# Kernel optimization log

Measured on AMD Instinct MI355X. Metric: run time of the kernel, lower is better.

## Reference

```python
import jax, jax.numpy as jnp
import numpy as np

B, N, E, F = 4, 4096, 65536, 128


def setup_inputs() -> dict:
    key = jax.random.key(0)
    ks = jax.random.split(key, 16)
    s = 0.02
    inp = {
        'node_feats': jax.random.normal(ks[0], (B, N, F), jnp.float32),
        'edge_feats': jax.random.normal(ks[1], (B, E, F), jnp.float32),
        'i': jax.random.randint(ks[2], (E,), 0, N, jnp.int32),
        'j': jax.random.randint(ks[3], (E,), 0, N, jnp.int32),
        'W_src_gate': jax.random.normal(ks[4], (F, F), jnp.float32) * s,
        'b_src_gate': jnp.zeros((F,), jnp.float32),
        'W_dst_gate': jax.random.normal(ks[5], (F, F), jnp.float32) * s,
        'b_dst_gate': jnp.zeros((F,), jnp.float32),
        'W_edge_gate': jax.random.normal(ks[6], (F, F), jnp.float32) * s,
        'b_edge_gate': jnp.zeros((F,), jnp.float32),
        'W_src_update': jax.random.normal(ks[7], (F, F), jnp.float32) * s,
        'b_src_update': jnp.zeros((F,), jnp.float32),
        'W_dst_update': jax.random.normal(ks[8], (F, F), jnp.float32) * s,
        'b_dst_update': jnp.zeros((F,), jnp.float32),
    }
    return inp


def _linear(x, W, b):
    # torch nn.Linear: x @ W.T + b, W is [out, in]
    return jnp.einsum('bnf,gf->bng', x, W) + b


def reference(node_feats, edge_feats, i, j,
              W_src_gate, b_src_gate, W_dst_gate, b_dst_gate,
              W_edge_gate, b_edge_gate, W_src_update, b_src_update,
              W_dst_update, b_dst_update):
    Bn, Nn, Fn = node_feats.shape
    e_src = _linear(node_feats, W_src_gate, b_src_gate)[:, i]      # [B, E, F]
    e_dst = _linear(node_feats, W_dst_gate, b_dst_gate)[:, j]      # [B, E, F]
    y = e_src + e_dst + _linear(edge_feats, W_edge_gate, b_edge_gate)
    sigma = jax.nn.sigmoid(y)
    bh = _linear(node_feats, W_dst_update, b_dst_update)[:, j]     # [B, E, F]
    m = bh * sigma
    # scatter-add over edges into destination nodes (along dim 1)
    zeros = jnp.zeros((Bn, Nn, Fn), node_feats.dtype)
    sum_sigma_h = zeros.at[:, i].add(m)
    sum_sigma = zeros.at[:, i].add(sigma)
    h = sum_sigma_h / (sum_sigma + 1e-6)
    x = jax.nn.silu(_linear(node_feats, W_src_update, b_src_update) + h)
    y = jax.nn.silu(y)
    # residual=True
    x = node_feats + x
    y = edge_feats + y
    return (x, y)
```

## Files before the change

kernel.cpp:

```cpp
#include <hip/hip_runtime.h>
#include <hip/hip_bf16.h>

typedef __attribute__((ext_vector_type(8))) short short8;
typedef __attribute__((ext_vector_type(4))) float f32x4;
typedef __attribute__((ext_vector_type(2))) float f32x2;

#define DEVI __device__ __forceinline__

static constexpr int NB = 4;
static constexpr int NN = 4096;
static constexpr int NE = 65536;
static constexpr int MROWS = NB * NN;

DEVI short f2b(float f) {
    __hip_bfloat16 h = __float2bfloat16(f);
    return *reinterpret_cast<short*>(&h);
}
DEVI float b2f(ushort u) {
    uint v = (uint)u << 16;
    float f;
    __builtin_memcpy(&f, &v, 4);
    return f;
}

__global__ void prep_weights(const float* __restrict__ w0, const float* __restrict__ w1,
                             const float* __restrict__ w2, const float* __restrict__ w3,
                             const float* __restrict__ w4, ushort* __restrict__ out) {
    int idx = blockIdx.x * 256 + threadIdx.x;
    int wsel = idx >> 14;
    int off = idx & 16383;
    const float* src = wsel == 0 ? w0 : wsel == 1 ? w1 : wsel == 2 ? w2 : wsel == 3 ? w3 : w4;
    out[idx] = (ushort)f2b(src[off]);
}

__global__ void hist_kernel(const int* __restrict__ iIdx, int* __restrict__ cnt) {
    int e = blockIdx.x * 256 + threadIdx.x;
    atomicAdd(&cnt[iIdx[e]], 1);
}

__global__ __launch_bounds__(256) void scan_kernel(const int* __restrict__ cnt,
                                                   int* __restrict__ start) {
    __shared__ int ls[256];
    int t = threadIdx.x;
    int base = t * 16;
    int loc[16];
    int s = 0;
#pragma unroll
    for (int q = 0; q < 16; ++q) { loc[q] = s; s += cnt[base + q]; }
    ls[t] = s;
    __syncthreads();
    for (int off = 1; off < 256; off <<= 1) {
        int v = (t >= off) ? ls[t - off] : 0;
        __syncthreads();
        ls[t] += v;
        __syncthreads();
    }
    int ex = ls[t] - s;
#pragma unroll
    for (int q = 0; q < 16; ++q) start[base + q] = ex + loc[q];
    if (t == 255) start[4096] = ex + s;
}

__global__ void scatter_kernel(const int* __restrict__ iIdx, const int* __restrict__ jIdx,
                               const int* __restrict__ start, int* __restrict__ cur,
                               int* __restrict__ rank, int* __restrict__ jsort) {
    int e = blockIdx.x * 256 + threadIdx.x;
    int iv = iIdx[e];
    int pos = start[iv] + atomicAdd(&cur[iv], 1);
    rank[e] = pos;
    jsort[pos] = jIdx[e];
}

DEVI void stage_W256(const ushort* __restrict__ Wg, ushort* Wl, int tid) {
    int n = tid >> 1;
    int kh = (tid & 1) * 64;
#pragma unroll
    for (int c = 0; c < 8; ++c) {
        int k = kh + c * 8;
        short8 v = *reinterpret_cast<const short8*>(Wg + n * 128 + k);
        int byt = (n * 256 + k * 2) ^ ((n & 7) << 4);
        *reinterpret_cast<short8*>(reinterpret_cast<char*>(Wl) + byt) = v;
    }
}

DEVI void stage_W512(const ushort* __restrict__ Wg, ushort* Wl, int tid) {
    int n = tid >> 2;
    int kq = (tid & 3) * 32;
#pragma unroll
    for (int c = 0; c < 4; ++c) {
        int k = kq + c * 8;
        short8 v = *reinterpret_cast<const short8*>(Wg + n * 128 + k);
        int byt = (n * 256 + k * 2) ^ ((n & 7) << 4);
        *reinterpret_cast<short8*>(reinterpret_cast<char*>(Wl) + byt) = v;
    }
}

DEVI void load_afrag(const float* __restrict__ rowptr, int kgrp, short8 afrag[4]) {
#pragma unroll
    for (int ks = 0; ks < 4; ++ks) {
        int k0 = ks * 32 + kgrp * 8;
        f32x4 lo = *reinterpret_cast<const f32x4*>(rowptr + k0);
        f32x4 hi = *reinterpret_cast<const f32x4*>(rowptr + k0 + 4);
        short8 a;
#pragma unroll
        for (int q = 0; q < 4; ++q) a[q] = f2b(lo[q]);
#pragma unroll
        for (int q = 0; q < 4; ++q) a[4 + q] = f2b(hi[q]);
        afrag[ks] = a;
    }
}

DEVI void mfma_frags(const short8 afrag[4], const ushort* __restrict__ Wl,
                     int lane, f32x4 acc[8]) {
    const int colb = lane & 15;
    const int kgrp = lane >> 4;
#pragma unroll
    for (int nt = 0; nt < 8; ++nt) acc[nt] = f32x4{0.f, 0.f, 0.f, 0.f};
#pragma unroll
    for (int ks = 0; ks < 4; ++ks) {
#pragma unroll
        for (int nt = 0; nt < 8; ++nt) {
            int n = nt * 16 + colb;
            int byt = (n * 256 + (ks * 32 + kgrp * 8) * 2) ^ ((n & 7) << 4);
            short8 bfrag = *reinterpret_cast<const short8*>(
                reinterpret_cast<const char*>(Wl) + byt);
            acc[nt] = __builtin_amdgcn_mfma_f32_16x16x32_bf16(afrag[ks], bfrag, acc[nt], 0, 0, 0);
        }
    }
}

__global__ __launch_bounds__(256) void node_proj_kernel(
    const float* __restrict__ node_feats,
    const ushort* __restrict__ Wbf,
    const float* __restrict__ bias0, const float* __restrict__ bias1,
    const float* __restrict__ bias2, const float* __restrict__ bias3,
    ushort* __restrict__ P)
{
    __shared__ ushort Wl[128 * 128];
    const int widx = blockIdx.y;
    const int row0 = blockIdx.x * 64;
    const int tid = threadIdx.x;

    stage_W256(Wbf + (size_t)widx * 16384, Wl, tid);
    __syncthreads();

    const int lane = tid & 63, wv = tid >> 6;
    const int colb = lane & 15, kgrp = lane >> 4;
    short8 afrag[4];
    load_afrag(node_feats + (size_t)(row0 + wv * 16 + colb) * 128, kgrp, afrag);
    f32x4 acc[8];
    mfma_frags(afrag, Wl, lane, acc);

    const float* bias = widx == 0 ? bias0 : widx == 1 ? bias1 : widx == 2 ? bias2 : bias3;
    ushort* Po = P + (size_t)widx * MROWS * 128;
#pragma unroll
    for (int r = 0; r < 4; ++r) {
        int row = row0 + wv * 16 + kgrp * 4 + r;
#pragma unroll
        for (int nt = 0; nt < 8; ++nt) {
            int col = nt * 16 + colb;
            Po[(size_t)row * 128 + col] = (ushort)f2b(acc[nt][r] + bias[col]);
        }
    }
}

__global__ __launch_bounds__(512, 4) void edge_kernel(
    const float* __restrict__ edge_feats,
    const int* __restrict__ iIdx, const int* __restrict__ jIdx,
    const int* __restrict__ rank,
    const ushort* __restrict__ Weg,
    const float* __restrict__ b_eg,
    const ushort* __restrict__ Psg, const ushort* __restrict__ Pdg,
    ushort* __restrict__ sigS,
    float* __restrict__ yOut)
{
    __shared__ ushort Wl[128 * 128];
    const int b = blockIdx.y;
    const int e0 = blockIdx.x * 128;
    const int tid = threadIdx.x;

    stage_W512(Weg, Wl, tid);
    __syncthreads();

    const int lane = tid & 63, wv = tid >> 6;
    const int colb = lane & 15, kgrp = lane >> 4;
    const float* Ab = edge_feats + (size_t)b * NE * 128;
    const size_t nbase = (size_t)b * NN;

    short8 afrag[4];
    load_afrag(Ab + (size_t)(e0 + wv * 16 + colb) * 128, kgrp, afrag);
    f32x4 acc[8];
    mfma_frags(afrag, Wl, lane, acc);

#pragma unroll
    for (int r = 0; r < 4; ++r) {
        int erow = wv * 16 + kgrp * 4 + r;
        int e = e0 + erow;
        int ie = iIdx[e], je = jIdx[e], rk = rank[e];
        const ushort* sg = Psg + (nbase + ie) * 128;
        const ushort* dg = Pdg + (nbase + je) * 128;
        const float* ef = Ab + (size_t)(e0 + erow) * 128;
        float* yo = yOut + ((size_t)b * NE + e) * 128;
        ushort* so = sigS + ((size_t)b * NE + rk) * 128;
#pragma unroll
        for (int nt = 0; nt < 8; ++nt) {
            int col = nt * 16 + colb;
            float y = acc[nt][r] + b_eg[col] + b2f(sg[col]) + b2f(dg[col]);
            float sig = 1.0f / (1.0f + __expf(-y));
            yo[col] = ef[col] + y * sig;
            so[col] = (ushort)f2b(sig);
        }
    }
}

__global__ __launch_bounds__(256) void node_reduce_kernel(
    const ushort* __restrict__ sigS,
    const int* __restrict__ start,
    const int* __restrict__ jsort,
    const ushort* __restrict__ Pdu,
    const ushort* __restrict__ Psu,
    const float* __restrict__ nf,
    float* __restrict__ xOut)
{
    int task = blockIdx.x * 4 + (threadIdx.x >> 6);
    int lane = threadIdx.x & 63;
    int b = task >> 12;
    int n = task & 4095;
    int s0 = start[n], s1 = start[n + 1];

    const size_t ebase = (size_t)b * NE;
    const size_t nbase = (size_t)b * NN;

    float S0 = 0.f, S1 = 0.f, Sh0 = 0.f, Sh1 = 0.f;
    int k = s0;
    for (; k + 2 <= s1; k += 2) {
        int ja = jsort[k], jb = jsort[k + 1];
        uint sa2 = *reinterpret_cast<const uint*>(sigS + (ebase + k) * 128 + lane * 2);
        uint sb2 = *reinterpret_cast<const uint*>(sigS + (ebase + k + 1) * 128 + lane * 2);
        uint da2 = *reinterpret_cast<const uint*>(Pdu + (nbase + ja) * 128 + lane * 2);
        uint db2 = *reinterpret_cast<const uint*>(Pdu + (nbase + jb) * 128 + lane * 2);
        float sa0 = b2f((ushort)(sa2 & 0xffff)), sa1 = b2f((ushort)(sa2 >> 16));
        float sb0 = b2f((ushort)(sb2 & 0xffff)), sb1 = b2f((ushort)(sb2 >> 16));
        float da0 = b2f((ushort)(da2 & 0xffff)), da1 = b2f((ushort)(da2 >> 16));
        float db0 = b2f((ushort)(db2 & 0xffff)), db1 = b2f((ushort)(db2 >> 16));
        S0 += sa0 + sb0; S1 += sa1 + sb1;
        Sh0 += da0 * sa0 + db0 * sb0;
        Sh1 += da1 * sa1 + db1 * sb1;
    }
    if (k < s1) {
        int j = jsort[k];
        uint sg2 = *reinterpret_cast<const uint*>(sigS + (ebase + k) * 128 + lane * 2);
        uint du2 = *reinterpret_cast<const uint*>(Pdu + (nbase + j) * 128 + lane * 2);
        float sa = b2f((ushort)(sg2 & 0xffff)), sb = b2f((ushort)(sg2 >> 16));
        float da = b2f((ushort)(du2 & 0xffff)), db = b2f((ushort)(du2 >> 16));
        S0 += sa; S1 += sb;
        Sh0 += da * sa; Sh1 += db * sb;
    }

    size_t off = (nbase + n) * 128 + lane * 2;
    uint su2 = *reinterpret_cast<const uint*>(Psu + off);
    f32x2 a = *reinterpret_cast<const f32x2*>(nf + off);
    float h0 = Sh0 / (S0 + 1e-6f);
    float h1 = Sh1 / (S1 + 1e-6f);
    float v0 = b2f((ushort)(su2 & 0xffff)) + h0;
    float v1 = b2f((ushort)(su2 >> 16)) + h1;
    f32x2 r;
    r[0] = a[0] + v0 / (1.f + __expf(-v0));
    r[1] = a[1] + v1 / (1.f + __expf(-v1));
    *reinterpret_cast<f32x2*>(xOut + off) = r;
}

extern "C" void kernel_launch(void* const* d_in, const int* in_sizes, int n_in,
                              void* d_out, int out_size, void* d_ws, size_t ws_size,
                              hipStream_t stream) {
    (void)in_sizes; (void)n_in; (void)out_size; (void)ws_size;

    const float* node_feats = (const float*)d_in[0];
    const float* edge_feats = (const float*)d_in[1];
    const int* iIdx = (const int*)d_in[2];
    const int* jIdx = (const int*)d_in[3];
    const float* Wsg = (const float*)d_in[4];  const float* bsg = (const float*)d_in[5];
    const float* Wdg = (const float*)d_in[6];  const float* bdg = (const float*)d_in[7];
    const float* Weg = (const float*)d_in[8];  const float* beg = (const float*)d_in[9];
    const float* Wsu = (const float*)d_in[10]; const float* bsu = (const float*)d_in[11];
    const float* Wdu = (const float*)d_in[12]; const float* bdu = (const float*)d_in[13];

    float* out = (float*)d_out;
    float* xOut = out;
    float* yOut = out + (size_t)MROWS * 128;

    ushort* sigS = (ushort*)d_ws;
    ushort* P = sigS + (size_t)NB * NE * 128;
    ushort* Wbf = P + (size_t)4 * MROWS * 128;
    int* rank = (int*)(Wbf + 5 * 16384);
    int* jsort = rank + NE;
    int* cnt = jsort + NE;
    int* cur = cnt + 4096;
    int* start = cur + 4096;

    hipMemsetAsync(cnt, 0, 2 * 4096 * sizeof(int), stream);

    prep_weights<<<(5 * 16384) / 256, 256, 0, stream>>>(Wsg, Wdg, Wdu, Wsu, Weg, Wbf);

    hist_kernel<<<NE / 256, 256, 0, stream>>>(iIdx, cnt);
    scan_kernel<<<1, 256, 0, stream>>>(cnt, start);
    scatter_kernel<<<NE / 256, 256, 0, stream>>>(iIdx, jIdx, start, cur, rank, jsort);

    dim3 gA(MROWS / 64, 4);
    node_proj_kernel<<<gA, 256, 0, stream>>>(node_feats, Wbf, bsg, bdg, bdu, bsu, P);

    dim3 gB(NE / 128, NB);
    edge_kernel<<<gB, 512, 0, stream>>>(edge_feats, iIdx, jIdx, rank,
                                        Wbf + (size_t)4 * 16384, beg,
                                        P,
                                        P + (size_t)1 * MROWS * 128,
                                        sigS, yOut);

    node_reduce_kernel<<<MROWS / 4, 256, 0, stream>>>(
        sigS, start, jsort,
        P + (size_t)2 * MROWS * 128,
        P + (size_t)3 * MROWS * 128,
        node_feats, xOut);
}
```

Baseline: 168.3 us.

## Write sigma in edge order and gather via permutation; loop weights in node_proj

The edge kernel now writes sigma contiguously in edge order instead of scattering each row to its sorted rank. The node reduce kernel reads sigma indirectly through a new perm array built by the scatter kernel. The node projection kernel now loads the A fragments once and loops over all four weight matrices, which cuts its grid from 4x to 1x over the node rows. The aim is coalesced writes in the edge kernel and no repeated node_feats reads. The cost is gathered, uncoalesced sigma reads in the reduction and a serial four-step loop with fewer blocks in node_proj.

```diff
diff --git a/kernel.cpp b/kernel.cpp
--- a/kernel.cpp
+++ b/kernel.cpp
@@ -63,11 +63,11 @@
 
 __global__ void scatter_kernel(const int* __restrict__ iIdx, const int* __restrict__ jIdx,
                                const int* __restrict__ start, int* __restrict__ cur,
-                               int* __restrict__ rank, int* __restrict__ jsort) {
+                               int* __restrict__ perm, int* __restrict__ jsort) {
     int e = blockIdx.x * 256 + threadIdx.x;
     int iv = iIdx[e];
     int pos = start[iv] + atomicAdd(&cur[iv], 1);
-    rank[e] = pos;
+    perm[pos] = e;
     jsort[pos] = jIdx[e];
 }
 
@@ -137,29 +137,32 @@
     ushort* __restrict__ P)
 {
     __shared__ ushort Wl[128 * 128];
-    const int widx = blockIdx.y;
     const int row0 = blockIdx.x * 64;
     const int tid = threadIdx.x;
-
-    stage_W256(Wbf + (size_t)widx * 16384, Wl, tid);
-    __syncthreads();
-
     const int lane = tid & 63, wv = tid >> 6;
     const int colb = lane & 15, kgrp = lane >> 4;
+
     short8 afrag[4];
     load_afrag(node_feats + (size_t)(row0 + wv * 16 + colb) * 128, kgrp, afrag);
-    f32x4 acc[8];
-    mfma_frags(afrag, Wl, lane, acc);
-
-    const float* bias = widx == 0 ? bias0 : widx == 1 ? bias1 : widx == 2 ? bias2 : bias3;
-    ushort* Po = P + (size_t)widx * MROWS * 128;
-#pragma unroll
-    for (int r = 0; r < 4; ++r) {
-        int row = row0 + wv * 16 + kgrp * 4 + r;
-#pragma unroll
-        for (int nt = 0; nt < 8; ++nt) {
-            int col = nt * 16 + colb;
-            Po[(size_t)row * 128 + col] = (ushort)f2b(acc[nt][r] + bias[col]);
+
+    const float* biases[4] = {bias0, bias1, bias2, bias3};
+#pragma unroll
+    for (int w = 0; w < 4; ++w) {
+        __syncthreads();
+        stage_W256(Wbf + (size_t)w * 16384, Wl, tid);
+        __syncthreads();
+        f32x4 acc[8];
+        mfma_frags(afrag, Wl, lane, acc);
+        const float* bias = biases[w];
+        ushort* Po = P + (size_t)w * MROWS * 128;
+#pragma unroll
+        for (int r = 0; r < 4; ++r) {
+            int row = row0 + wv * 16 + kgrp * 4 + r;
+#pragma unroll
+            for (int nt = 0; nt < 8; ++nt) {
+                int col = nt * 16 + colb;
+                Po[(size_t)row * 128 + col] = (ushort)f2b(acc[nt][r] + bias[col]);
+            }
         }
     }
 }
@@ -167,11 +170,10 @@
 __global__ __launch_bounds__(512, 4) void edge_kernel(
     const float* __restrict__ edge_feats,
     const int* __restrict__ iIdx, const int* __restrict__ jIdx,
-    const int* __restrict__ rank,
     const ushort* __restrict__ Weg,
     const float* __restrict__ b_eg,
     const ushort* __restrict__ Psg, const ushort* __restrict__ Pdg,
-    ushort* __restrict__ sigS,
+    ushort* __restrict__ sigma,
     float* __restrict__ yOut)
 {
     __shared__ ushort Wl[128 * 128];
@@ -196,12 +198,12 @@
     for (int r = 0; r < 4; ++r) {
         int erow = wv * 16 + kgrp * 4 + r;
         int e = e0 + erow;
-        int ie = iIdx[e], je = jIdx[e], rk = rank[e];
+        int ie = iIdx[e], je = jIdx[e];
         const ushort* sg = Psg + (nbase + ie) * 128;
         const ushort* dg = Pdg + (nbase + je) * 128;
         const float* ef = Ab + (size_t)(e0 + erow) * 128;
         float* yo = yOut + ((size_t)b * NE + e) * 128;
-        ushort* so = sigS + ((size_t)b * NE + rk) * 128;
+        ushort* so = sigma + ((size_t)b * NE + e) * 128;
 #pragma unroll
         for (int nt = 0; nt < 8; ++nt) {
             int col = nt * 16 + colb;
@@ -214,7 +216,8 @@
 }
 
 __global__ __launch_bounds__(256) void node_reduce_kernel(
-    const ushort* __restrict__ sigS,
+    const ushort* __restrict__ sigma,
+    const int* __restrict__ perm,
     const int* __restrict__ start,
     const int* __restrict__ jsort,
     const ushort* __restrict__ Pdu,
@@ -234,9 +237,10 @@
     float S0 = 0.f, S1 = 0.f, Sh0 = 0.f, Sh1 = 0.f;
     int k = s0;
     for (; k + 2 <= s1; k += 2) {
+        int ea = perm[k], eb = perm[k + 1];
         int ja = jsort[k], jb = jsort[k + 1];
-        uint sa2 = *reinterpret_cast<const uint*>(sigS + (ebase + k) * 128 + lane * 2);
-        uint sb2 = *reinterpret_cast<const uint*>(sigS + (ebase + k + 1) * 128 + lane * 2);
+        uint sa2 = *reinterpret_cast<const uint*>(sigma + (ebase + ea) * 128 + lane * 2);
+        uint sb2 = *reinterpret_cast<const uint*>(sigma + (ebase + eb) * 128 + lane * 2);
         uint da2 = *reinterpret_cast<const uint*>(Pdu + (nbase + ja) * 128 + lane * 2);
         uint db2 = *reinterpret_cast<const uint*>(Pdu + (nbase + jb) * 128 + lane * 2);
         float sa0 = b2f((ushort)(sa2 & 0xffff)), sa1 = b2f((ushort)(sa2 >> 16));
@@ -248,8 +252,9 @@
         Sh1 += da1 * sa1 + db1 * sb1;
     }
     if (k < s1) {
+        int e = perm[k];
         int j = jsort[k];
-        uint sg2 = *reinterpret_cast<const uint*>(sigS + (ebase + k) * 128 + lane * 2);
+        uint sg2 = *reinterpret_cast<const uint*>(sigma + (ebase + e) * 128 + lane * 2);
         uint du2 = *reinterpret_cast<const uint*>(Pdu + (nbase + j) * 128 + lane * 2);
         float sa = b2f((ushort)(sg2 & 0xffff)), sb = b2f((ushort)(sg2 >> 16));
         float da = b2f((ushort)(du2 & 0xffff)), db = b2f((ushort)(du2 >> 16));
@@ -289,11 +294,11 @@
     float* xOut = out;
     float* yOut = out + (size_t)MROWS * 128;
 
-    ushort* sigS = (ushort*)d_ws;
-    ushort* P = sigS + (size_t)NB * NE * 128;
+    ushort* sigma = (ushort*)d_ws;
+    ushort* P = sigma + (size_t)NB * NE * 128;
     ushort* Wbf = P + (size_t)4 * MROWS * 128;
-    int* rank = (int*)(Wbf + 5 * 16384);
-    int* jsort = rank + NE;
+    int* perm = (int*)(Wbf + 5 * 16384);
+    int* jsort = perm + NE;
     int* cnt = jsort + NE;
     int* cur = cnt + 4096;
     int* start = cur + 4096;
@@ -304,20 +309,19 @@
 
     hist_kernel<<<NE / 256, 256, 0, stream>>>(iIdx, cnt);
     scan_kernel<<<1, 256, 0, stream>>>(cnt, start);
-    scatter_kernel<<<NE / 256, 256, 0, stream>>>(iIdx, jIdx, start, cur, rank, jsort);
-
-    dim3 gA(MROWS / 64, 4);
-    node_proj_kernel<<<gA, 256, 0, stream>>>(node_feats, Wbf, bsg, bdg, bdu, bsu, P);
+    scatter_kernel<<<NE / 256, 256, 0, stream>>>(iIdx, jIdx, start, cur, perm, jsort);
+
+    node_proj_kernel<<<MROWS / 64, 256, 0, stream>>>(node_feats, Wbf, bsg, bdg, bdu, bsu, P);
 
     dim3 gB(NE / 128, NB);
-    edge_kernel<<<gB, 512, 0, stream>>>(edge_feats, iIdx, jIdx, rank,
+    edge_kernel<<<gB, 512, 0, stream>>>(edge_feats, iIdx, jIdx,
                                         Wbf + (size_t)4 * 16384, beg,
                                         P,
                                         P + (size_t)1 * MROWS * 128,
-                                        sigS, yOut);
+                                        sigma, yOut);
 
     node_reduce_kernel<<<MROWS / 4, 256, 0, stream>>>(
-        sigS, start, jsort,
+        sigma, perm, start, jsort,
         P + (size_t)2 * MROWS * 128,
         P + (size_t)3 * MROWS * 128,
         node_feats, xOut);
```

After: 171.7 us. 1.02x slower.
